# Kernel tuning notes

Hardware: AMD Instinct MI355X
Metric: run time of the kernel (lower is better)

Reference implementation:

```python
import jax, jax.numpy as jnp
import numpy as np

NB, HD, NL, NF = 5, 64, 4, 10           # num_bins, hidden_dim(d_model), num_layers, num_frames
DI, DS, DC, DTR = 128, 16, 4, 4          # d_inner=2*HD, d_state, d_conv, dt_rank=ceil(HD/16)
B, H, W = 4, 64, 64


def _conv2d(x, w, b):
    y = jax.lax.conv_general_dilated(x, w, (1, 1), 'SAME',
                                     dimension_numbers=('NCHW', 'OIHW', 'NCHW'))
    return y + b[None, :, None, None]


def _bn_relu(x, gamma, beta, eps=1e-5):
    # BatchNorm2d in training mode: biased batch stats over (N,H,W)
    mean = x.mean(axis=(0, 2, 3), keepdims=True)
    var = x.var(axis=(0, 2, 3), keepdims=True)
    y = (x - mean) * jax.lax.rsqrt(var + eps)
    return jax.nn.relu(y * gamma[None, :, None, None] + beta[None, :, None, None])


def _silu(x):
    return x * jax.nn.sigmoid(x)


def _causal_dwconv(x, w, b):
    # x: (B,L,DI), w: (DI,K) depthwise causal conv, b: (DI,)
    K = w.shape[1]
    L = x.shape[1]
    xp = jnp.pad(x, ((0, 0), (K - 1, 0), (0, 0)))
    y = sum(xp[:, k:k + L, :] * w[:, k] for k in range(K))
    return y + b


def _selective_scan(u, delta, A, Bm, Cm, D):
    # u,delta: (B,L,DI); A: (DI,DS); Bm,Cm: (B,L,DS); D: (DI,)
    dT, BT, CT, uT = (t.transpose(1, 0, 2) for t in (delta, Bm, Cm, u))
    h0 = jnp.zeros((u.shape[0], A.shape[0], A.shape[1]), u.dtype)

    def step(h, inp):
        d_t, B_t, C_t, u_t = inp                     # (B,DI),(B,DS),(B,DS),(B,DI)
        dA = jnp.exp(d_t[:, :, None] * A)            # (B,DI,DS)
        h = dA * h + (d_t * u_t)[:, :, None] * B_t[:, None, :]
        y = jnp.einsum('bds,bs->bd', h, C_t)
        return h, y

    _, ys = jax.lax.scan(step, h0, (dT, BT, CT, uT))  # ys: (L,B,DI)
    return ys.transpose(1, 0, 2) + u * D


def _mamba(x, in_proj, conv_w, conv_b, x_proj, dt_w, dt_b, A_log, Dp, out_proj):
    xz = x @ in_proj.T                               # (B,L,2*DI)
    xi, z = jnp.split(xz, 2, axis=-1)
    xi = _silu(_causal_dwconv(xi, conv_w, conv_b))
    xdbc = xi @ x_proj.T                             # (B,L,DTR+2*DS)
    dt, Bm, Cm = jnp.split(xdbc, [DTR, DTR + DS], axis=-1)
    delta = jax.nn.softplus(dt @ dt_w.T + dt_b)
    A = -jnp.exp(A_log)
    y = _selective_scan(xi, delta, A, Bm, Cm, Dp)
    return (y * _silu(z)) @ out_proj.T


def setup_inputs() -> dict:
    key = jax.random.key(0)
    ks = jax.random.split(key, 20)
    s = 0.02
    inp = {
        'x': jax.random.normal(ks[0], (B, NB, H, W), jnp.float32),
        'enc_w': jax.random.normal(ks[1], (HD, NB, 3, 3), jnp.float32) * s,
        'enc_b': jnp.zeros((HD,), jnp.float32),
        'enc_g': jnp.ones((HD,), jnp.float32),
        'enc_be': jnp.zeros((HD,), jnp.float32),
        'in_proj': jax.random.normal(ks[2], (NL, 2 * DI, HD), jnp.float32) * s,
        'conv_w': jax.random.normal(ks[3], (NL, DI, DC), jnp.float32) * s,
        'conv_b': jnp.zeros((NL, DI), jnp.float32),
        'x_proj': jax.random.normal(ks[4], (NL, DTR + 2 * DS, DI), jnp.float32) * s,
        'dt_w': jax.random.normal(ks[5], (NL, DI, DTR), jnp.float32) * s,
        'dt_b': jax.random.normal(ks[6], (NL, DI), jnp.float32) * 0.1 - 4.0,
        'A_log': jnp.broadcast_to(jnp.log(jnp.arange(1, DS + 1, dtype=jnp.float32)),
                                  (NL, DI, DS)).copy(),
        'Dp': jnp.ones((NL, DI), jnp.float32),
        'out_proj': jax.random.normal(ks[7], (NL, HD, DI), jnp.float32) * s,
        'dec1_w': jax.random.normal(ks[8], (HD, HD, 3, 3), jnp.float32) * s,
        'dec1_b': jnp.zeros((HD,), jnp.float32),
        'dec1_g': jnp.ones((HD,), jnp.float32),
        'dec1_be': jnp.zeros((HD,), jnp.float32),
        'dec2_w': jax.random.normal(ks[9], (NF, HD, 3, 3), jnp.float32) * s,
        'dec2_b': jnp.zeros((NF,), jnp.float32),
    }
    return inp


def reference(x, enc_w, enc_b, enc_g, enc_be, in_proj, conv_w, conv_b, x_proj,
              dt_w, dt_b, A_log, Dp, out_proj, dec1_w, dec1_b, dec1_g, dec1_be,
              dec2_w, dec2_b):
    Bb, _, Hh, Ww = x.shape
    h = _bn_relu(_conv2d(x, enc_w, enc_b), enc_g, enc_be)   # (B,HD,H,W)
    t = h.reshape(Bb, HD, Hh * Ww).transpose(0, 2, 1)        # (B,L,HD)
    for i in range(NL):
        t = t + _mamba(t, in_proj[i], conv_w[i], conv_b[i], x_proj[i],
                       dt_w[i], dt_b[i], A_log[i], Dp[i], out_proj[i])
    h = t.transpose(0, 2, 1).reshape(Bb, HD, Hh, Ww)
    h = _bn_relu(_conv2d(h, dec1_w, dec1_b), dec1_g, dec1_be)
    return _conv2d(h, dec2_w, dec2_b)                        # (B,NF,H,W)
```

## Files before the change

kernel.cpp:

```cpp
#include <hip/hip_runtime.h>
#include <hip/hip_bf16.h>

#define BB   4
#define NBC  5
#define HD   64
#define NLAYER 4
#define NFC  10
#define DIM  128
#define DSN  16
#define DCN  4
#define DTRK 4
#define HH   64
#define WWD  64
#define LL   4096
#define MM   (BB*LL)
#define NCHUNK 128
#define CLEN   32

__global__ void k_prep_all(const float* __restrict__ in_proj, const float* __restrict__ out_proj,
                           const float* __restrict__ dec1_w, const float* __restrict__ dec2_w,
                           float* __restrict__ wTin, float* __restrict__ wTout,
                           float* __restrict__ wT1, float* __restrict__ wT2,
                           float* __restrict__ stats, float* __restrict__ stats2) {
    int idx = blockIdx.x * blockDim.x + threadIdx.x;
    if (idx < 65536) {
        int n = idx & 255, k = (idx >> 8) & 63, l = idx >> 14;
        wTin[idx] = in_proj[(l << 14) + (n << 6) + k];
    } else if (idx < 98304) {
        int j = idx - 65536;
        int n = j & 63, k = (j >> 6) & 127, l = j >> 13;
        wTout[j] = out_proj[(l << 13) + (n << 7) + k];
    } else if (idx < 135168) {
        int j = idx - 98304;
        int co = j & 63, tap = (j >> 6) % 9, ci = j / 576;
        wT1[j] = dec1_w[co * 576 + ci * 9 + tap];
    } else if (idx < 142848) {
        int j = idx - 135168;
        int tap = j % 12, t2 = j / 12, co = t2 % NFC, ci = t2 / NFC;
        wT2[j] = (tap < 9) ? dec2_w[co * 576 + ci * 9 + tap] : 0.f;
    } else if (idx < 143104) {
        int j = idx - 142848;
        if (j < 128) stats[j] = 0.f; else stats2[j - 128] = 0.f;
    }
}

__global__ void k_enc_conv(const float* __restrict__ x, const float* __restrict__ w,
                           const float* __restrict__ bias, float* __restrict__ out,
                           float* __restrict__ stats) {
    __shared__ float r1[256], r2[256];
    int tid = threadIdx.x;
    int idx = blockIdx.x * 256 + tid;
    int wx = idx & 63;
    int hy = (idx >> 6) & 63;
    int co = (idx >> 12) & 63;
    int b  = idx >> 18;
    float acc = bias[co];
    for (int ci = 0; ci < NBC; ++ci) {
        const float* xin = x + (((long)(b * NBC + ci)) << 12);
        const float* wp  = w + (co * NBC + ci) * 9;
        #pragma unroll
        for (int kh = 0; kh < 3; ++kh) {
            int ih = hy + kh - 1;
            if (ih < 0 || ih >= HH) continue;
            #pragma unroll
            for (int kw = 0; kw < 3; ++kw) {
                int iw = wx + kw - 1;
                if (iw < 0 || iw >= WWD) continue;
                acc += xin[(ih << 6) + iw] * wp[kh * 3 + kw];
            }
        }
    }
    out[idx] = acc;
    r1[tid] = acc; r2[tid] = acc * acc;
    __syncthreads();
    for (int off = 128; off > 0; off >>= 1) {
        if (tid < off) { r1[tid] += r1[tid + off]; r2[tid] += r2[tid + off]; }
        __syncthreads();
    }
    if (tid == 0) {
        atomicAdd(&stats[co], r1[0]);
        atomicAdd(&stats[64 + co], r2[0]);
    }
}

__global__ __launch_bounds__(256, 1) void k_gemm_in_bn(const float* __restrict__ src,
                                                       const float* __restrict__ stats,
                                                       const float* __restrict__ g,
                                                       const float* __restrict__ be,
                                                       const float* __restrict__ wT,
                                                       float* __restrict__ tout,
                                                       float* __restrict__ xz) {
    __shared__ __align__(16) float ts[64 * 68];
    __shared__ float sc[64], sh[64];
    long m0 = (long)blockIdx.x << 6;
    int b = (int)(m0 >> 12);
    int hw0 = (int)(m0 & 4095);
    int tid = threadIdx.x;
    if (tid < 64) {
        float m = stats[tid] * (1.f / 16384.f);
        float var = stats[64 + tid] * (1.f / 16384.f) - m * m;
        float ss = g[tid] * rsqrtf(var + 1e-5f);
        sc[tid] = ss; sh[tid] = be[tid] - m * ss;
    }
    __syncthreads();
    for (int i = tid; i < 4096; i += 256) {
        int pix = i & 63, c = i >> 6;
        float v = src[(((long)((b << 6) + c)) << 12) + hw0 + pix];
        ts[pix * 68 + c] = fmaxf(v * sc[c] + sh[c], 0.f);
    }
    __syncthreads();
    for (int i = tid; i < 4096; i += 256) {
        int r = i >> 6, c = i & 63;
        tout[(m0 + r) * 64 + c] = ts[r * 68 + c];
    }
    int rg = tid >> 5;
    int cg = tid & 31;
    float acc[8][8] = {};
    int n0 = cg << 3;
    for (int k4 = 0; k4 < 16; ++k4) {
        float4 a[8];
        #pragma unroll
        for (int r2 = 0; r2 < 8; ++r2)
            a[r2] = *(const float4*)&ts[((rg << 3) + r2) * 68 + (k4 << 2)];
        #pragma unroll
        for (int kk = 0; kk < 4; ++kk) {
            const float* wr = wT + (((k4 << 2) + kk) << 8) + n0;
            float4 w0 = *(const float4*)&wr[0];
            float4 w1 = *(const float4*)&wr[4];
            #pragma unroll
            for (int r2 = 0; r2 < 8; ++r2) {
                float av = (kk == 0) ? a[r2].x : (kk == 1) ? a[r2].y
                         : (kk == 2) ? a[r2].z : a[r2].w;
                acc[r2][0] += av * w0.x; acc[r2][1] += av * w0.y;
                acc[r2][2] += av * w0.z; acc[r2][3] += av * w0.w;
                acc[r2][4] += av * w1.x; acc[r2][5] += av * w1.y;
                acc[r2][6] += av * w1.z; acc[r2][7] += av * w1.w;
            }
        }
    }
    #pragma unroll
    for (int r2 = 0; r2 < 8; ++r2) {
        long m = m0 + (rg << 3) + r2;
        *(float4*)&xz[(m << 8) + n0]     = make_float4(acc[r2][0], acc[r2][1], acc[r2][2], acc[r2][3]);
        *(float4*)&xz[(m << 8) + n0 + 4] = make_float4(acc[r2][4], acc[r2][5], acc[r2][6], acc[r2][7]);
    }
}

__global__ __launch_bounds__(256, 2) void k_xproj_fused(
        const float* __restrict__ xz, const float* __restrict__ cw,
        const float* __restrict__ cb, const float* __restrict__ Wx,
        const float* __restrict__ dw, const float* __restrict__ dbias,
        const float* __restrict__ A_log,
        float* __restrict__ xi, float* __restrict__ xdbc,
        float* __restrict__ delta, float* __restrict__ Pb, float* __restrict__ Sb) {
    __shared__ float xz_s[35 * 132];
    __shared__ float xi_s[32 * 132];
    __shared__ float w_s[36 * 132];
    __shared__ float xs[32 * 40];
    __shared__ float cwT[4 * 128];
    __shared__ float cb_s[128];
    long m0 = (long)blockIdx.x << 5;
    int l0 = (int)(m0 & 4095);
    int b = (int)(m0 >> 12);
    int chunk = l0 >> 5;
    int tid = threadIdx.x;

    for (int i = tid; i < 35 * 128; i += 256) {
        int j = i >> 7, k = i & 127;
        int l = l0 - 3 + j;
        float v = 0.f;
        if (l >= 0) v = xz[(m0 - 3 + j) * 256 + k];
        xz_s[j * 132 + k] = v;
    }
    if (tid < 128) cb_s[tid] = cb[tid];
    for (int i = tid; i < 512; i += 256) {
        int kk = i >> 7, di = i & 127;
        cwT[(kk << 7) + di] = cw[(di << 2) + kk];
    }
    for (int i = tid; i < 4608; i += 256) {
        int n = i >> 7, k = i & 127;
        w_s[n * 132 + k] = Wx[i];
    }
    __syncthreads();

    for (int ii = 0; ii < 4; ++ii) {
        int i = tid + (ii << 8);
        int r = i >> 5;
        int d4 = (i & 31) << 2;
        float4 a = *(const float4*)&cb_s[d4];
        #pragma unroll
        for (int kk = 0; kk < 4; ++kk) {
            float4 xv = *(const float4*)&xz_s[(r + kk) * 132 + d4];
            float4 wv = *(const float4*)&cwT[(kk << 7) + d4];
            a.x += xv.x * wv.x; a.y += xv.y * wv.y;
            a.z += xv.z * wv.z; a.w += xv.w * wv.w;
        }
        a.x = a.x / (1.f + __expf(-a.x));
        a.y = a.y / (1.f + __expf(-a.y));
        a.z = a.z / (1.f + __expf(-a.z));
        a.w = a.w / (1.f + __expf(-a.w));
        *(float4*)&xi_s[r * 132 + d4] = a;
        *(float4*)&xi[(m0 + r) * 128 + d4] = a;
    }
    __syncthreads();

    int n = tid & 63;
    int rg = tid >> 6;
    if (n < 36) {
        float acc[8] = {0,0,0,0,0,0,0,0};
        for (int k4 = 0; k4 < 32; ++k4) {
            float4 w4 = *(const float4*)&w_s[n * 132 + (k4 << 2)];
            #pragma unroll
            for (int r = 0; r < 8; ++r) {
                float4 a4 = *(const float4*)&xi_s[((rg << 3) + r) * 132 + (k4 << 2)];
                acc[r] += a4.x * w4.x + a4.y * w4.y + a4.z * w4.z + a4.w * w4.w;
            }
        }
        #pragma unroll
        for (int r = 0; r < 8; ++r) {
            int rr = (rg << 3) + r;
            xdbc[(m0 + rr) * 36 + n] = acc[r];
            xs[rr * 40 + n] = acc[r];
        }
    }
    __syncthreads();

    float* delta_s = xz_s;
    for (int i = tid; i < 4096; i += 256) {
        int r = i >> 7, di = i & 127;
        float v = dbias[di];
        float4 d4 = *(const float4*)&dw[di << 2];
        v += xs[r * 40 + 0] * d4.x + xs[r * 40 + 1] * d4.y
           + xs[r * 40 + 2] * d4.z + xs[r * 40 + 3] * d4.w;
        float sp = (v > 20.f) ? v : log1pf(expf(v));
        delta[(m0 + r) * 128 + di] = sp;
        delta_s[r * 132 + di] = sp;
    }
    __syncthreads();

    {
        int di = tid >> 1;
        int dso = (tid & 1) << 3;
        float4 al0 = *(const float4*)&A_log[(di << 4) + dso];
        float4 al1 = *(const float4*)&A_log[(di << 4) + dso + 4];
        float Av[8] = { -expf(al0.x), -expf(al0.y), -expf(al0.z), -expf(al0.w),
                        -expf(al1.x), -expf(al1.y), -expf(al1.z), -expf(al1.w) };
        float h[8] = {0,0,0,0,0,0,0,0};
        float P[8] = {1,1,1,1,1,1,1,1};
        #pragma unroll 4
        for (int i = 0; i < CLEN; ++i) {
            float d = delta_s[i * 132 + di];
            float u = xi_s[i * 132 + di];
            float du = d * u;
            float4 B0 = *(float4*)&xs[i * 40 + DTRK + dso];
            float4 B1 = *(float4*)&xs[i * 40 + DTRK + dso + 4];
            float a0 = __expf(d * Av[0]); h[0] = a0 * h[0] + du * B0.x; P[0] *= a0;
            float a1 = __expf(d * Av[1]); h[1] = a1 * h[1] + du * B0.y; P[1] *= a1;
            float a2 = __expf(d * Av[2]); h[2] = a2 * h[2] + du * B0.z; P[2] *= a2;
            float a3 = __expf(d * Av[3]); h[3] = a3 * h[3] + du * B0.w; P[3] *= a3;
            float a4 = __expf(d * Av[4]); h[4] = a4 * h[4] + du * B1.x; P[4] *= a4;
            float a5 = __expf(d * Av[5]); h[5] = a5 * h[5] + du * B1.y; P[5] *= a5;
            float a6 = __expf(d * Av[6]); h[6] = a6 * h[6] + du * B1.z; P[6] *= a6;
            float a7 = __expf(d * Av[7]); h[7] = a7 * h[7] + du * B1.w; P[7] *= a7;
        }
        long o = (((long)chunk * BB + b) << 11) + (di << 4) + dso;
        *(float4*)&Pb[o]     = make_float4(P[0], P[1], P[2], P[3]);
        *(float4*)&Pb[o + 4] = make_float4(P[4], P[5], P[6], P[7]);
        *(float4*)&Sb[o]     = make_float4(h[0], h[1], h[2], h[3]);
        *(float4*)&Sb[o + 4] = make_float4(h[4], h[5], h[6], h[7]);
    }
}

__global__ void k_scan_p2(float* Pb, const float* __restrict__ Sb) {
    int t = blockIdx.x * blockDim.x + threadIdx.x;
    int b = t >> 11;
    int s = t & 2047;
    float h = 0.f;
    for (int c = 0; c < NCHUNK; ++c) {
        long idx = (((long)c * BB + b) << 11) + s;
        float p = Pb[idx];
        float sv = Sb[idx];
        Pb[idx] = h;
        h = p * h + sv;
    }
}

__global__ __launch_bounds__(256, 1) void k_scan_p3_oi(
        const float* __restrict__ delta, const float* __restrict__ xi,
        const float* __restrict__ xdbc, const float* __restrict__ A_log,
        const float* __restrict__ Dp, const float* __restrict__ xz,
        const float* __restrict__ hin, const float* __restrict__ wTo,
        const float* __restrict__ wTi, float* __restrict__ tio,
        float* __restrict__ xz_out, int doB) {
    __shared__ __align__(16) float d_s[32 * 132];
    __shared__ __align__(16) float u_s[32 * 132];
    __shared__ __align__(16) float bc_s[32 * 36];
    __shared__ __align__(16) float t_s[32 * 68];
    int chunk = blockIdx.x, b = blockIdx.y;
    int tid = threadIdx.x;
    long t0 = ((long)b << 12) + (long)chunk * CLEN;

    for (int i = tid; i < 1024; i += 256) {
        int r = i >> 5, c4 = (i & 31) << 2;
        *(float4*)&d_s[r * 132 + c4] = *(const float4*)&delta[(t0 + r) * 128 + c4];
        *(float4*)&u_s[r * 132 + c4] = *(const float4*)&xi[(t0 + r) * 128 + c4];
    }
    {
        int r = tid >> 3, c4 = (tid & 7) << 2;
        *(float4*)&bc_s[r * 36 + c4] = *(const float4*)&xdbc[(t0 + r) * 36 + DTRK + c4];
    }

    int di = tid >> 1;
    int dso = (tid & 1) << 3;
    float4 al0 = *(const float4*)&A_log[(di << 4) + dso];
    float4 al1 = *(const float4*)&A_log[(di << 4) + dso + 4];
    float Av[8] = { -expf(al0.x), -expf(al0.y), -expf(al0.z), -expf(al0.w),
                    -expf(al1.x), -expf(al1.y), -expf(al1.z), -expf(al1.w) };
    float Dv = Dp[di];
    long o = (((long)chunk * BB + b) << 11) + (di << 4) + dso;
    float4 h0 = *(const float4*)&hin[o];
    float4 h1 = *(const float4*)&hin[o + 4];
    float h[8] = { h0.x, h0.y, h0.z, h0.w, h1.x, h1.y, h1.z, h1.w };
    __syncthreads();

    #pragma unroll 4
    for (int i = 0; i < CLEN; ++i) {
        float d = d_s[i * 132 + di];
        float u = u_s[i * 132 + di];
        float du = d * u;
        const float* bc = &bc_s[i * 36];
        float4 B0 = *(const float4*)&bc[dso];
        float4 B1 = *(const float4*)&bc[dso + 4];
        float4 C0 = *(const float4*)&bc[16 + dso];
        float4 C1 = *(const float4*)&bc[16 + dso + 4];
        float a0 = __expf(d * Av[0]); h[0] = a0 * h[0] + du * B0.x;
        float a1 = __expf(d * Av[1]); h[1] = a1 * h[1] + du * B0.y;
        float a2 = __expf(d * Av[2]); h[2] = a2 * h[2] + du * B0.z;
        float a3 = __expf(d * Av[3]); h[3] = a3 * h[3] + du * B0.w;
        float a4 = __expf(d * Av[4]); h[4] = a4 * h[4] + du * B1.x;
        float a5 = __expf(d * Av[5]); h[5] = a5 * h[5] + du * B1.y;
        float a6 = __expf(d * Av[6]); h[6] = a6 * h[6] + du * B1.z;
        float a7 = __expf(d * Av[7]); h[7] = a7 * h[7] + du * B1.w;
        float yp = h[0] * C0.x + h[1] * C0.y + h[2] * C0.z + h[3] * C0.w
                 + h[4] * C1.x + h[5] * C1.y + h[6] * C1.z + h[7] * C1.w;
        yp += __shfl_xor(yp, 1);
        if (dso == 0)
            u_s[i * 132 + di] = yp + u * Dv;
    }
    __syncthreads();

    for (int i = tid; i < 1024; i += 256) {
        int r = i >> 5, c4 = (i & 31) << 2;
        float4 y4 = *(float4*)&u_s[r * 132 + c4];
        float4 z4 = *(const float4*)&xz[((t0 + r) << 8) + DIM + c4];
        y4.x *= z4.x / (1.f + __expf(-z4.x));
        y4.y *= z4.y / (1.f + __expf(-z4.y));
        y4.z *= z4.z / (1.f + __expf(-z4.z));
        y4.w *= z4.w / (1.f + __expf(-z4.w));
        *(float4*)&u_s[r * 132 + c4] = y4;
    }
    __syncthreads();

    {
        int rg = tid >> 4, cg = tid & 15;
        int n0 = cg << 2;
        float acc[2][4] = {};
        for (int k4 = 0; k4 < 32; ++k4) {
            float4 a0 = *(const float4*)&u_s[(rg << 1) * 132 + (k4 << 2)];
            float4 a1 = *(const float4*)&u_s[((rg << 1) + 1) * 132 + (k4 << 2)];
            #pragma unroll
            for (int kk = 0; kk < 4; ++kk) {
                const float* wr = wTo + (((k4 << 2) + kk) << 6) + n0;
                float4 w0 = *(const float4*)&wr[0];
                float av0 = (kk == 0) ? a0.x : (kk == 1) ? a0.y : (kk == 2) ? a0.z : a0.w;
                float av1 = (kk == 0) ? a1.x : (kk == 1) ? a1.y : (kk == 2) ? a1.z : a1.w;
                acc[0][0] += av0 * w0.x; acc[0][1] += av0 * w0.y;
                acc[0][2] += av0 * w0.z; acc[0][3] += av0 * w0.w;
                acc[1][0] += av1 * w0.x; acc[1][1] += av1 * w0.y;
                acc[1][2] += av1 * w0.z; acc[1][3] += av1 * w0.w;
            }
        }
        #pragma unroll
        for (int r2 = 0; r2 < 2; ++r2) {
            long m = t0 + (rg << 1) + r2;
            float4 tv = *(const float4*)&tio[(m << 6) + n0];
            tv.x += acc[r2][0]; tv.y += acc[r2][1];
            tv.z += acc[r2][2]; tv.w += acc[r2][3];
            *(float4*)&tio[(m << 6) + n0] = tv;
            *(float4*)&t_s[((rg << 1) + r2) * 68 + n0] = tv;
        }
    }
    if (!doB) return;
    __syncthreads();

    {
        int rg = tid >> 5, cgn = tid & 31;
        int n0 = cgn << 3;
        float acc[4][8] = {};
        for (int k4 = 0; k4 < 16; ++k4) {
            float4 a[4];
            #pragma unroll
            for (int r2 = 0; r2 < 4; ++r2)
                a[r2] = *(const float4*)&t_s[((rg << 2) + r2) * 68 + (k4 << 2)];
            #pragma unroll
            for (int kk = 0; kk < 4; ++kk) {
                const float* wr = wTi + (((k4 << 2) + kk) << 8) + n0;
                float4 w0 = *(const float4*)&wr[0];
                float4 w1 = *(const float4*)&wr[4];
                #pragma unroll
                for (int r2 = 0; r2 < 4; ++r2) {
                    float av = (kk == 0) ? a[r2].x : (kk == 1) ? a[r2].y
                             : (kk == 2) ? a[r2].z : a[r2].w;
                    acc[r2][0] += av * w0.x; acc[r2][1] += av * w0.y;
                    acc[r2][2] += av * w0.z; acc[r2][3] += av * w0.w;
                    acc[r2][4] += av * w1.x; acc[r2][5] += av * w1.y;
                    acc[r2][6] += av * w1.z; acc[r2][7] += av * w1.w;
                }
            }
        }
        #pragma unroll
        for (int r2 = 0; r2 < 4; ++r2) {
            long m = t0 + (rg << 2) + r2;
            *(float4*)&xz_out[(m << 8) + n0]     = make_float4(acc[r2][0], acc[r2][1], acc[r2][2], acc[r2][3]);
            *(float4*)&xz_out[(m << 8) + n0 + 4] = make_float4(acc[r2][4], acc[r2][5], acc[r2][6], acc[r2][7]);
        }
    }
}

__global__ __launch_bounds__(256, 1) void k_dec1_new(const float* __restrict__ tin,
                                                     const float* __restrict__ wT,
                                                     const float* __restrict__ bias,
                                                     float* __restrict__ out,
                                                     float* __restrict__ stats2) {
    __shared__ __align__(16) float x_s[64 * 132];
    __shared__ __align__(16) float w_s[4 * 4608];
    int tile = blockIdx.x;
    int b = blockIdx.y;
    int ty0 = (tile >> 3) << 3;
    int tx0 = (tile & 7) << 3;
    int tid = threadIdx.x;
    int wv = tid >> 6;
    int lane = tid & 63;
    int r = lane >> 3;
    int cg = lane & 7;

    for (int i = tid; i < 6400; i += 256) {
        int pl = i >> 6;
        int c = i & 63;
        int py = pl / 10, px = pl - py * 10;
        int ih = ty0 + py - 1, iw = tx0 + px - 1;
        float v = 0.f;
        if (ih >= 0 && ih < HH && iw >= 0 && iw < WWD)
            v = tin[(((long)((b << 12) + (ih << 6) + iw)) << 6) + c];
        x_s[c * 132 + py * 12 + px] = v;
    }
    float* myw = &w_s[wv * 4608];
    const float* gw = wT + (wv * 16) * 576;
    float4 pref[18];
    #pragma unroll
    for (int i = 0; i < 18; ++i)
        pref[i] = *(const float4*)&gw[(i * 64 + lane) * 4];
    #pragma unroll
    for (int i = 0; i < 18; ++i)
        *(float4*)&myw[(i * 64 + lane) * 4] = pref[i];
    __syncthreads();

    float acc[8][8] = {};
    #pragma unroll
    for (int ch = 0; ch < 2; ++ch) {
        if (ch == 0) {
            const float* gw1 = wT + (wv * 16 + 8) * 576;
            #pragma unroll
            for (int i = 0; i < 18; ++i)
                pref[i] = *(const float4*)&gw1[(i * 64 + lane) * 4];
        }
        for (int cl = 0; cl < 8; ++cl) {
            int cib = wv * 16 + ch * 8 + cl;
            float xrow[3][10];
            #pragma unroll
            for (int kh = 0; kh < 3; ++kh) {
                const float* xr = &x_s[cib * 132 + (r + kh) * 12];
                float4 a0 = *(const float4*)&xr[0];
                float4 a1 = *(const float4*)&xr[4];
                float2 a2 = *(const float2*)&xr[8];
                xrow[kh][0] = a0.x; xrow[kh][1] = a0.y; xrow[kh][2] = a0.z; xrow[kh][3] = a0.w;
                xrow[kh][4] = a1.x; xrow[kh][5] = a1.y; xrow[kh][6] = a1.z; xrow[kh][7] = a1.w;
                xrow[kh][8] = a2.x; xrow[kh][9] = a2.y;
            }
            const float* wp = &myw[cl * 576];
            #pragma unroll
            for (int kh = 0; kh < 3; ++kh) {
                #pragma unroll
                for (int kw = 0; kw < 3; ++kw) {
                    const float* wp2 = wp + (kh * 3 + kw) * 64 + (cg << 3);
                    float4 wa = *(const float4*)&wp2[0];
                    float4 wb = *(const float4*)&wp2[4];
                    #pragma unroll
                    for (int j = 0; j < 8; ++j) {
                        float xv = xrow[kh][kw + j];
                        acc[j][0] += xv * wa.x; acc[j][1] += xv * wa.y;
                        acc[j][2] += xv * wa.z; acc[j][3] += xv * wa.w;
                        acc[j][4] += xv * wb.x; acc[j][5] += xv * wb.y;
                        acc[j][6] += xv * wb.z; acc[j][7] += xv * wb.w;
                    }
                }
            }
        }
        if (ch == 0) {
            #pragma unroll
            for (int i = 0; i < 18; ++i)
                *(float4*)&myw[(i * 64 + lane) * 4] = pref[i];
        }
    }

    #pragma unroll
    for (int j = 0; j < 8; ++j) {
        *(float4*)&myw[lane * 68 + (j << 3)]     = make_float4(acc[j][0], acc[j][1], acc[j][2], acc[j][3]);
        *(float4*)&myw[lane * 68 + (j << 3) + 4] = make_float4(acc[j][4], acc[j][5], acc[j][6], acc[j][7]);
    }
    __syncthreads();

    float bv = bias[lane];
    float ssum = 0.f, ssq = 0.f;
    #pragma unroll
    for (int pp = 0; pp < 16; ++pp) {
        int pr = (wv << 1) + (pp >> 3);
        int pc = pp & 7;
        int ol = (pr << 3) + (lane >> 3);
        int ix = (pc << 3) + (lane & 7);
        float s = w_s[ol * 68 + ix] + w_s[4608 + ol * 68 + ix]
                + w_s[9216 + ol * 68 + ix] + w_s[13824 + ol * 68 + ix] + bv;
        out[(((long)((b << 12) + ((ty0 + pr) << 6) + tx0 + pc)) << 6) + lane] = s;
        ssum += s; ssq += s * s;
    }
    float* red = x_s;
    red[(wv << 6) + lane] = ssum;
    red[256 + (wv << 6) + lane] = ssq;
    __syncthreads();
    if (tid < 64) {
        float a = red[tid] + red[64 + tid] + red[128 + tid] + red[192 + tid];
        float q = red[256 + tid] + red[320 + tid] + red[384 + tid] + red[448 + tid];
        atomicAdd(&stats2[tid], a);
        atomicAdd(&stats2[64 + tid], q);
    }
}

__global__ void k_dec2_fused(const float* __restrict__ src, const float* __restrict__ stats2,
                             const float* __restrict__ g, const float* __restrict__ be,
                             const float* __restrict__ wT, const float* __restrict__ bias,
                             float* __restrict__ out) {
    __shared__ float x_s[64 * 101];
    __shared__ float w_s[64 * NFC * 12];
    __shared__ float sc_s[64];
    __shared__ float sh_s[64];
    int tile = blockIdx.x;
    int b = blockIdx.y;
    int ty0 = (tile >> 3) << 3;
    int tx0 = (tile & 7) << 3;
    int tid = threadIdx.x;

    if (tid < 64) {
        float m = stats2[tid] * (1.f / 16384.f);
        float var = stats2[64 + tid] * (1.f / 16384.f) - m * m;
        float s = g[tid] * rsqrtf(var + 1e-5f);
        sc_s[tid] = s;
        sh_s[tid] = be[tid] - m * s;
    }
    for (int i = tid; i < 64 * NFC * 12; i += 256)
        w_s[i] = wT[i];
    __syncthreads();

    for (int i = tid; i < 6400; i += 256) {
        int pl = i >> 6;
        int c = i & 63;
        int py = pl / 10, px = pl - py * 10;
        int ih = ty0 + py - 1, iw = tx0 + px - 1;
        float v = 0.f;
        if (ih >= 0 && ih < HH && iw >= 0 && iw < WWD) {
            v = src[((long)((b << 12) + (ih << 6) + iw)) * 64 + c];
            v = fmaxf(v * sc_s[c] + sh_s[c], 0.f);
        }
        x_s[c * 101 + pl] = v;
    }
    __syncthreads();

    int px = tid & 63;
    int py = px >> 3, pxx = px & 7;
    int cog = tid >> 6;
    float acc[3] = {0.f, 0.f, 0.f};
    int nco = (cog < 2) ? 3 : 2;

    for (int ci = 0; ci < 64; ++ci) {
        const float* xr = &x_s[ci * 101 + py * 10 + pxx];
        float xv[9];
        #pragma unroll
        for (int kh = 0; kh < 3; ++kh)
            #pragma unroll
            for (int kw = 0; kw < 3; ++kw)
                xv[kh * 3 + kw] = xr[kh * 10 + kw];
        #pragma unroll
        for (int j = 0; j < 3; ++j) {
            if (j >= nco) break;
            int co = cog + (j << 2);
            const float* wp = &w_s[(ci * NFC + co) * 12];
            float4 w0 = *(const float4*)&wp[0];
            float4 w1 = *(const float4*)&wp[4];
            float  w8 = wp[8];
            acc[j] += xv[0] * w0.x + xv[1] * w0.y + xv[2] * w0.z + xv[3] * w0.w
                    + xv[4] * w1.x + xv[5] * w1.y + xv[6] * w1.z + xv[7] * w1.w
                    + xv[8] * w8;
        }
    }
    int hw = ((ty0 + py) << 6) + tx0 + pxx;
    #pragma unroll
    for (int j = 0; j < 3; ++j) {
        if (j >= nco) break;
        int co = cog + (j << 2);
        out[((long)(b * NFC + co) << 12) + hw] = acc[j] + bias[co];
    }
}

extern "C" void kernel_launch(void* const* d_in, const int* in_sizes, int n_in,
                              void* d_out, int out_size, void* d_ws, size_t ws_size,
                              hipStream_t stream) {
    const float* x       = (const float*)d_in[0];
    const float* enc_w   = (const float*)d_in[1];
    const float* enc_b   = (const float*)d_in[2];
    const float* enc_g   = (const float*)d_in[3];
    const float* enc_be  = (const float*)d_in[4];
    const float* in_proj = (const float*)d_in[5];
    const float* conv_w  = (const float*)d_in[6];
    const float* conv_b  = (const float*)d_in[7];
    const float* x_proj  = (const float*)d_in[8];
    const float* dt_w    = (const float*)d_in[9];
    const float* dt_b    = (const float*)d_in[10];
    const float* A_log   = (const float*)d_in[11];
    const float* Dp      = (const float*)d_in[12];
    const float* out_prj = (const float*)d_in[13];
    const float* dec1_w  = (const float*)d_in[14];
    const float* dec1_b  = (const float*)d_in[15];
    const float* dec1_g  = (const float*)d_in[16];
    const float* dec1_be = (const float*)d_in[17];
    const float* dec2_w  = (const float*)d_in[18];
    const float* dec2_b  = (const float*)d_in[19];
    float* out = (float*)d_out;

    float* ws = (float*)d_ws;
    size_t off = 0;
    float* conv_buf  = ws + off; off += 1048576;
    float* stats     = ws + off; off += 128;
    float* stats2    = ws + off; off += 128;
    float* wT1       = ws + off; off += 36864;
    float* wT2       = ws + off; off += 7680;
    float* wTin      = ws + off; off += 65536;
    float* wTout     = ws + off; off += 32768;
    float* t_buf     = ws + off; off += 1048576;
    float* xz_buf    = ws + off; off += 4194304;
    float* xi_buf    = ws + off; off += 2097152;
    float* xdbc_buf  = ws + off; off += 589824;
    float* delta_buf = ws + off; off += 2097152;
    float* Sb_buf    = ws + off; off += 1048576;
    (void)ws_size; (void)in_sizes; (void)n_in; (void)out_size;

    float* Pb = conv_buf;
    float* Sb = Sb_buf;

    k_prep_all<<<560, 256, 0, stream>>>(in_proj, out_prj, dec1_w, dec2_w,
                                        wTin, wTout, wT1, wT2, stats, stats2);

    k_enc_conv<<<4096, 256, 0, stream>>>(x, enc_w, enc_b, conv_buf, stats);

    k_gemm_in_bn<<<256, 256, 0, stream>>>(conv_buf, stats, enc_g, enc_be, wTin, t_buf, xz_buf);
    dim3 pg(NCHUNK, BB);
    for (int i = 0; i < NLAYER; ++i) {
        k_xproj_fused<<<512, 256, 0, stream>>>(xz_buf, conv_w + i * DIM * DCN,
                                               conv_b + i * DIM, x_proj + i * 36 * DIM,
                                               dt_w + i * DIM * DTRK, dt_b + i * DIM,
                                               A_log + i * DIM * DSN,
                                               xi_buf, xdbc_buf, delta_buf, Pb, Sb);
        k_scan_p2<<<32, 256, 0, stream>>>(Pb, Sb);
        int doB = (i < NLAYER - 1) ? 1 : 0;
        k_scan_p3_oi<<<pg, 256, 0, stream>>>(delta_buf, xi_buf, xdbc_buf,
                                             A_log + i * DIM * DSN, Dp + i * DIM,
                                             xz_buf, Pb, wTout + i * 8192,
                                             wTin + ((i + 1) & 3) * 16384,
                                             t_buf, xz_buf, doB);
    }

    dim3 dg1(64, BB);
    k_dec1_new<<<dg1, 256, 0, stream>>>(t_buf, wT1, dec1_b, conv_buf, stats2);
    k_dec2_fused<<<dg1, 256, 0, stream>>>(conv_buf, stats2, dec1_g, dec1_be, wT2, dec2_b, out);
}
```

Measured before the change: 491.8 us.

## Fuse all Mamba layers into one persistent cooperative kernel with grid syncs

Replaces the per-layer three-kernel sequence (xproj+chunk scan, inter-chunk scan, output scan+projections) with a single cooperative kernel of 512 blocks that loops over the four layers and separates phases with grid-wide syncs. Each block keeps its chunk's xi, delta and B/C values in shared memory across phases instead of writing xi/delta/xdbc to global memory and re-reading them. This removes kernel launch overhead and global round trips. In exchange it relies on all 512 blocks being co-resident (two per CU at 256 threads), and the sequential inter-chunk scan now runs on only 32 blocks while the rest wait at a grid barrier.

```diff
diff --git a/kernel.cpp b/kernel.cpp
--- a/kernel.cpp
+++ b/kernel.cpp
@@ -1,5 +1,8 @@
 #include <hip/hip_runtime.h>
 #include <hip/hip_bf16.h>
+#include <hip/hip_cooperative_groups.h>
+
+namespace cg = cooperative_groups;
 
 #define BB   4
 #define NBC  5
@@ -146,283 +149,266 @@
     }
 }
 
-__global__ __launch_bounds__(256, 2) void k_xproj_fused(
-        const float* __restrict__ xz, const float* __restrict__ cw,
-        const float* __restrict__ cb, const float* __restrict__ Wx,
-        const float* __restrict__ dw, const float* __restrict__ dbias,
-        const float* __restrict__ A_log,
-        float* __restrict__ xi, float* __restrict__ xdbc,
-        float* __restrict__ delta, float* __restrict__ Pb, float* __restrict__ Sb) {
-    __shared__ float xz_s[35 * 132];
-    __shared__ float xi_s[32 * 132];
-    __shared__ float w_s[36 * 132];
-    __shared__ float xs[32 * 40];
-    __shared__ float cwT[4 * 128];
-    __shared__ float cb_s[128];
-    long m0 = (long)blockIdx.x << 5;
+__global__ __launch_bounds__(256, 2) void k_mamba_all(
+        float* __restrict__ xz,
+        const float* __restrict__ cw_all, const float* __restrict__ cb_all,
+        const float* __restrict__ Wx_all,
+        const float* __restrict__ dw_all, const float* __restrict__ dbias_all,
+        const float* __restrict__ Alog_all, const float* __restrict__ Dp_all,
+        const float* __restrict__ wTo_all, const float* __restrict__ wTi_all,
+        float* __restrict__ tio, float* Pb, float* Sb) {
+    cg::grid_group gg = cg::this_grid();
+    __shared__ __align__(16) float smem[15516];
+    float* xz_s = smem;
+    float* xi_s = smem + 4620;
+    float* w_s  = smem + 8844;
+    float* xs   = smem + 13596;
+    float* cwT  = smem + 14876;
+    float* cb_s = smem + 15388;
+
+    int bx = blockIdx.x;
+    int tid = threadIdx.x;
+    long m0 = (long)bx << 5;
     int l0 = (int)(m0 & 4095);
-    int b = (int)(m0 >> 12);
-    int chunk = l0 >> 5;
-    int tid = threadIdx.x;
-
-    for (int i = tid; i < 35 * 128; i += 256) {
-        int j = i >> 7, k = i & 127;
-        int l = l0 - 3 + j;
-        float v = 0.f;
-        if (l >= 0) v = xz[(m0 - 3 + j) * 256 + k];
-        xz_s[j * 132 + k] = v;
-    }
-    if (tid < 128) cb_s[tid] = cb[tid];
-    for (int i = tid; i < 512; i += 256) {
-        int kk = i >> 7, di = i & 127;
-        cwT[(kk << 7) + di] = cw[(di << 2) + kk];
-    }
-    for (int i = tid; i < 4608; i += 256) {
-        int n = i >> 7, k = i & 127;
-        w_s[n * 132 + k] = Wx[i];
-    }
-    __syncthreads();
-
-    for (int ii = 0; ii < 4; ++ii) {
-        int i = tid + (ii << 8);
-        int r = i >> 5;
-        int d4 = (i & 31) << 2;
-        float4 a = *(const float4*)&cb_s[d4];
-        #pragma unroll
-        for (int kk = 0; kk < 4; ++kk) {
-            float4 xv = *(const float4*)&xz_s[(r + kk) * 132 + d4];
-            float4 wv = *(const float4*)&cwT[(kk << 7) + d4];
-            a.x += xv.x * wv.x; a.y += xv.y * wv.y;
-            a.z += xv.z * wv.z; a.w += xv.w * wv.w;
-        }
-        a.x = a.x / (1.f + __expf(-a.x));
-        a.y = a.y / (1.f + __expf(-a.y));
-        a.z = a.z / (1.f + __expf(-a.z));
-        a.w = a.w / (1.f + __expf(-a.w));
-        *(float4*)&xi_s[r * 132 + d4] = a;
-        *(float4*)&xi[(m0 + r) * 128 + d4] = a;
-    }
-    __syncthreads();
-
-    int n = tid & 63;
-    int rg = tid >> 6;
-    if (n < 36) {
-        float acc[8] = {0,0,0,0,0,0,0,0};
-        for (int k4 = 0; k4 < 32; ++k4) {
-            float4 w4 = *(const float4*)&w_s[n * 132 + (k4 << 2)];
-            #pragma unroll
-            for (int r = 0; r < 8; ++r) {
-                float4 a4 = *(const float4*)&xi_s[((rg << 3) + r) * 132 + (k4 << 2)];
-                acc[r] += a4.x * w4.x + a4.y * w4.y + a4.z * w4.z + a4.w * w4.w;
-            }
-        }
-        #pragma unroll
-        for (int r = 0; r < 8; ++r) {
-            int rr = (rg << 3) + r;
-            xdbc[(m0 + rr) * 36 + n] = acc[r];
-            xs[rr * 40 + n] = acc[r];
-        }
-    }
-    __syncthreads();
-
+    int b = bx >> 7;
+    int chunk = bx & 127;
+    int di = tid >> 1;
+    int dso = (tid & 1) << 3;
     float* delta_s = xz_s;
-    for (int i = tid; i < 4096; i += 256) {
-        int r = i >> 7, di = i & 127;
-        float v = dbias[di];
-        float4 d4 = *(const float4*)&dw[di << 2];
-        v += xs[r * 40 + 0] * d4.x + xs[r * 40 + 1] * d4.y
-           + xs[r * 40 + 2] * d4.z + xs[r * 40 + 3] * d4.w;
-        float sp = (v > 20.f) ? v : log1pf(expf(v));
-        delta[(m0 + r) * 128 + di] = sp;
-        delta_s[r * 132 + di] = sp;
-    }
-    __syncthreads();
-
-    {
-        int di = tid >> 1;
-        int dso = (tid & 1) << 3;
+
+    for (int L = 0; L < NLAYER; ++L) {
+        const float* cw    = cw_all + L * DIM * DCN;
+        const float* cbp   = cb_all + L * DIM;
+        const float* Wx    = Wx_all + L * 36 * DIM;
+        const float* dw    = dw_all + L * DIM * DTRK;
+        const float* dbias = dbias_all + L * DIM;
+        const float* A_log = Alog_all + L * DIM * DSN;
+        const float* wTo   = wTo_all + L * 8192;
+        const float* wTi   = wTi_all + ((L + 1) & 3) * 16384;
+
+        for (int i = tid; i < 35 * 128; i += 256) {
+            int j = i >> 7, k = i & 127;
+            int l = l0 - 3 + j;
+            float v = 0.f;
+            if (l >= 0) v = xz[(m0 - 3 + j) * 256 + k];
+            xz_s[j * 132 + k] = v;
+        }
+        if (tid < 128) cb_s[tid] = cbp[tid];
+        for (int i = tid; i < 512; i += 256) {
+            int kk = i >> 7, dd = i & 127;
+            cwT[(kk << 7) + dd] = cw[(dd << 2) + kk];
+        }
+        for (int i = tid; i < 4608; i += 256) {
+            int nn = i >> 7, k = i & 127;
+            w_s[nn * 132 + k] = Wx[i];
+        }
+        __syncthreads();
+
+        for (int ii = 0; ii < 4; ++ii) {
+            int i = tid + (ii << 8);
+            int r = i >> 5;
+            int d4 = (i & 31) << 2;
+            float4 a = *(const float4*)&cb_s[d4];
+            #pragma unroll
+            for (int kk = 0; kk < 4; ++kk) {
+                float4 xv = *(const float4*)&xz_s[(r + kk) * 132 + d4];
+                float4 wv = *(const float4*)&cwT[(kk << 7) + d4];
+                a.x += xv.x * wv.x; a.y += xv.y * wv.y;
+                a.z += xv.z * wv.z; a.w += xv.w * wv.w;
+            }
+            a.x = a.x / (1.f + __expf(-a.x));
+            a.y = a.y / (1.f + __expf(-a.y));
+            a.z = a.z / (1.f + __expf(-a.z));
+            a.w = a.w / (1.f + __expf(-a.w));
+            *(float4*)&xi_s[r * 132 + d4] = a;
+        }
+        __syncthreads();
+
+        {
+            int n = tid & 63;
+            int rg = tid >> 6;
+            if (n < 36) {
+                float acc[8] = {0,0,0,0,0,0,0,0};
+                for (int k4 = 0; k4 < 32; ++k4) {
+                    float4 w4 = *(const float4*)&w_s[n * 132 + (k4 << 2)];
+                    #pragma unroll
+                    for (int r = 0; r < 8; ++r) {
+                        float4 a4 = *(const float4*)&xi_s[((rg << 3) + r) * 132 + (k4 << 2)];
+                        acc[r] += a4.x * w4.x + a4.y * w4.y + a4.z * w4.z + a4.w * w4.w;
+                    }
+                }
+                #pragma unroll
+                for (int r = 0; r < 8; ++r)
+                    xs[((rg << 3) + r) * 40 + n] = acc[r];
+            }
+        }
+        __syncthreads();
+
+        for (int i = tid; i < 4096; i += 256) {
+            int r = i >> 7, dd = i & 127;
+            float v = dbias[dd];
+            float4 d4 = *(const float4*)&dw[dd << 2];
+            v += xs[r * 40 + 0] * d4.x + xs[r * 40 + 1] * d4.y
+               + xs[r * 40 + 2] * d4.z + xs[r * 40 + 3] * d4.w;
+            delta_s[r * 132 + dd] = (v > 20.f) ? v : log1pf(expf(v));
+        }
+        __syncthreads();
+
         float4 al0 = *(const float4*)&A_log[(di << 4) + dso];
         float4 al1 = *(const float4*)&A_log[(di << 4) + dso + 4];
         float Av[8] = { -expf(al0.x), -expf(al0.y), -expf(al0.z), -expf(al0.w),
                         -expf(al1.x), -expf(al1.y), -expf(al1.z), -expf(al1.w) };
-        float h[8] = {0,0,0,0,0,0,0,0};
-        float P[8] = {1,1,1,1,1,1,1,1};
-        #pragma unroll 4
-        for (int i = 0; i < CLEN; ++i) {
-            float d = delta_s[i * 132 + di];
-            float u = xi_s[i * 132 + di];
-            float du = d * u;
-            float4 B0 = *(float4*)&xs[i * 40 + DTRK + dso];
-            float4 B1 = *(float4*)&xs[i * 40 + DTRK + dso + 4];
-            float a0 = __expf(d * Av[0]); h[0] = a0 * h[0] + du * B0.x; P[0] *= a0;
-            float a1 = __expf(d * Av[1]); h[1] = a1 * h[1] + du * B0.y; P[1] *= a1;
-            float a2 = __expf(d * Av[2]); h[2] = a2 * h[2] + du * B0.z; P[2] *= a2;
-            float a3 = __expf(d * Av[3]); h[3] = a3 * h[3] + du * B0.w; P[3] *= a3;
-            float a4 = __expf(d * Av[4]); h[4] = a4 * h[4] + du * B1.x; P[4] *= a4;
-            float a5 = __expf(d * Av[5]); h[5] = a5 * h[5] + du * B1.y; P[5] *= a5;
-            float a6 = __expf(d * Av[6]); h[6] = a6 * h[6] + du * B1.z; P[6] *= a6;
-            float a7 = __expf(d * Av[7]); h[7] = a7 * h[7] + du * B1.w; P[7] *= a7;
-        }
         long o = (((long)chunk * BB + b) << 11) + (di << 4) + dso;
-        *(float4*)&Pb[o]     = make_float4(P[0], P[1], P[2], P[3]);
-        *(float4*)&Pb[o + 4] = make_float4(P[4], P[5], P[6], P[7]);
-        *(float4*)&Sb[o]     = make_float4(h[0], h[1], h[2], h[3]);
-        *(float4*)&Sb[o + 4] = make_float4(h[4], h[5], h[6], h[7]);
-    }
-}
-
-__global__ void k_scan_p2(float* Pb, const float* __restrict__ Sb) {
-    int t = blockIdx.x * blockDim.x + threadIdx.x;
-    int b = t >> 11;
-    int s = t & 2047;
-    float h = 0.f;
-    for (int c = 0; c < NCHUNK; ++c) {
-        long idx = (((long)c * BB + b) << 11) + s;
-        float p = Pb[idx];
-        float sv = Sb[idx];
-        Pb[idx] = h;
-        h = p * h + sv;
-    }
-}
-
-__global__ __launch_bounds__(256, 1) void k_scan_p3_oi(
-        const float* __restrict__ delta, const float* __restrict__ xi,
-        const float* __restrict__ xdbc, const float* __restrict__ A_log,
-        const float* __restrict__ Dp, const float* __restrict__ xz,
-        const float* __restrict__ hin, const float* __restrict__ wTo,
-        const float* __restrict__ wTi, float* __restrict__ tio,
-        float* __restrict__ xz_out, int doB) {
-    __shared__ __align__(16) float d_s[32 * 132];
-    __shared__ __align__(16) float u_s[32 * 132];
-    __shared__ __align__(16) float bc_s[32 * 36];
-    __shared__ __align__(16) float t_s[32 * 68];
-    int chunk = blockIdx.x, b = blockIdx.y;
-    int tid = threadIdx.x;
-    long t0 = ((long)b << 12) + (long)chunk * CLEN;
-
-    for (int i = tid; i < 1024; i += 256) {
-        int r = i >> 5, c4 = (i & 31) << 2;
-        *(float4*)&d_s[r * 132 + c4] = *(const float4*)&delta[(t0 + r) * 128 + c4];
-        *(float4*)&u_s[r * 132 + c4] = *(const float4*)&xi[(t0 + r) * 128 + c4];
-    }
-    {
-        int r = tid >> 3, c4 = (tid & 7) << 2;
-        *(float4*)&bc_s[r * 36 + c4] = *(const float4*)&xdbc[(t0 + r) * 36 + DTRK + c4];
-    }
-
-    int di = tid >> 1;
-    int dso = (tid & 1) << 3;
-    float4 al0 = *(const float4*)&A_log[(di << 4) + dso];
-    float4 al1 = *(const float4*)&A_log[(di << 4) + dso + 4];
-    float Av[8] = { -expf(al0.x), -expf(al0.y), -expf(al0.z), -expf(al0.w),
-                    -expf(al1.x), -expf(al1.y), -expf(al1.z), -expf(al1.w) };
-    float Dv = Dp[di];
-    long o = (((long)chunk * BB + b) << 11) + (di << 4) + dso;
-    float4 h0 = *(const float4*)&hin[o];
-    float4 h1 = *(const float4*)&hin[o + 4];
-    float h[8] = { h0.x, h0.y, h0.z, h0.w, h1.x, h1.y, h1.z, h1.w };
-    __syncthreads();
-
-    #pragma unroll 4
-    for (int i = 0; i < CLEN; ++i) {
-        float d = d_s[i * 132 + di];
-        float u = u_s[i * 132 + di];
-        float du = d * u;
-        const float* bc = &bc_s[i * 36];
-        float4 B0 = *(const float4*)&bc[dso];
-        float4 B1 = *(const float4*)&bc[dso + 4];
-        float4 C0 = *(const float4*)&bc[16 + dso];
-        float4 C1 = *(const float4*)&bc[16 + dso + 4];
-        float a0 = __expf(d * Av[0]); h[0] = a0 * h[0] + du * B0.x;
-        float a1 = __expf(d * Av[1]); h[1] = a1 * h[1] + du * B0.y;
-        float a2 = __expf(d * Av[2]); h[2] = a2 * h[2] + du * B0.z;
-        float a3 = __expf(d * Av[3]); h[3] = a3 * h[3] + du * B0.w;
-        float a4 = __expf(d * Av[4]); h[4] = a4 * h[4] + du * B1.x;
-        float a5 = __expf(d * Av[5]); h[5] = a5 * h[5] + du * B1.y;
-        float a6 = __expf(d * Av[6]); h[6] = a6 * h[6] + du * B1.z;
-        float a7 = __expf(d * Av[7]); h[7] = a7 * h[7] + du * B1.w;
-        float yp = h[0] * C0.x + h[1] * C0.y + h[2] * C0.z + h[3] * C0.w
-                 + h[4] * C1.x + h[5] * C1.y + h[6] * C1.z + h[7] * C1.w;
-        yp += __shfl_xor(yp, 1);
-        if (dso == 0)
-            u_s[i * 132 + di] = yp + u * Dv;
-    }
-    __syncthreads();
-
-    for (int i = tid; i < 1024; i += 256) {
-        int r = i >> 5, c4 = (i & 31) << 2;
-        float4 y4 = *(float4*)&u_s[r * 132 + c4];
-        float4 z4 = *(const float4*)&xz[((t0 + r) << 8) + DIM + c4];
-        y4.x *= z4.x / (1.f + __expf(-z4.x));
-        y4.y *= z4.y / (1.f + __expf(-z4.y));
-        y4.z *= z4.z / (1.f + __expf(-z4.z));
-        y4.w *= z4.w / (1.f + __expf(-z4.w));
-        *(float4*)&u_s[r * 132 + c4] = y4;
-    }
-    __syncthreads();
-
-    {
-        int rg = tid >> 4, cg = tid & 15;
-        int n0 = cg << 2;
-        float acc[2][4] = {};
-        for (int k4 = 0; k4 < 32; ++k4) {
-            float4 a0 = *(const float4*)&u_s[(rg << 1) * 132 + (k4 << 2)];
-            float4 a1 = *(const float4*)&u_s[((rg << 1) + 1) * 132 + (k4 << 2)];
-            #pragma unroll
-            for (int kk = 0; kk < 4; ++kk) {
-                const float* wr = wTo + (((k4 << 2) + kk) << 6) + n0;
-                float4 w0 = *(const float4*)&wr[0];
-                float av0 = (kk == 0) ? a0.x : (kk == 1) ? a0.y : (kk == 2) ? a0.z : a0.w;
-                float av1 = (kk == 0) ? a1.x : (kk == 1) ? a1.y : (kk == 2) ? a1.z : a1.w;
-                acc[0][0] += av0 * w0.x; acc[0][1] += av0 * w0.y;
-                acc[0][2] += av0 * w0.z; acc[0][3] += av0 * w0.w;
-                acc[1][0] += av1 * w0.x; acc[1][1] += av1 * w0.y;
-                acc[1][2] += av1 * w0.z; acc[1][3] += av1 * w0.w;
-            }
-        }
-        #pragma unroll
-        for (int r2 = 0; r2 < 2; ++r2) {
-            long m = t0 + (rg << 1) + r2;
-            float4 tv = *(const float4*)&tio[(m << 6) + n0];
-            tv.x += acc[r2][0]; tv.y += acc[r2][1];
-            tv.z += acc[r2][2]; tv.w += acc[r2][3];
-            *(float4*)&tio[(m << 6) + n0] = tv;
-            *(float4*)&t_s[((rg << 1) + r2) * 68 + n0] = tv;
-        }
-    }
-    if (!doB) return;
-    __syncthreads();
-
-    {
-        int rg = tid >> 5, cgn = tid & 31;
-        int n0 = cgn << 3;
-        float acc[4][8] = {};
-        for (int k4 = 0; k4 < 16; ++k4) {
-            float4 a[4];
-            #pragma unroll
-            for (int r2 = 0; r2 < 4; ++r2)
-                a[r2] = *(const float4*)&t_s[((rg << 2) + r2) * 68 + (k4 << 2)];
-            #pragma unroll
-            for (int kk = 0; kk < 4; ++kk) {
-                const float* wr = wTi + (((k4 << 2) + kk) << 8) + n0;
-                float4 w0 = *(const float4*)&wr[0];
-                float4 w1 = *(const float4*)&wr[4];
+
+        {
+            float h[8] = {0,0,0,0,0,0,0,0};
+            float P[8] = {1,1,1,1,1,1,1,1};
+            #pragma unroll 4
+            for (int i = 0; i < CLEN; ++i) {
+                float d = delta_s[i * 132 + di];
+                float u = xi_s[i * 132 + di];
+                float du = d * u;
+                float4 B0 = *(float4*)&xs[i * 40 + 4 + dso];
+                float4 B1 = *(float4*)&xs[i * 40 + 8 + dso];
+                float a0 = __expf(d * Av[0]); h[0] = a0 * h[0] + du * B0.x; P[0] *= a0;
+                float a1 = __expf(d * Av[1]); h[1] = a1 * h[1] + du * B0.y; P[1] *= a1;
+                float a2 = __expf(d * Av[2]); h[2] = a2 * h[2] + du * B0.z; P[2] *= a2;
+                float a3 = __expf(d * Av[3]); h[3] = a3 * h[3] + du * B0.w; P[3] *= a3;
+                float a4 = __expf(d * Av[4]); h[4] = a4 * h[4] + du * B1.x; P[4] *= a4;
+                float a5 = __expf(d * Av[5]); h[5] = a5 * h[5] + du * B1.y; P[5] *= a5;
+                float a6 = __expf(d * Av[6]); h[6] = a6 * h[6] + du * B1.z; P[6] *= a6;
+                float a7 = __expf(d * Av[7]); h[7] = a7 * h[7] + du * B1.w; P[7] *= a7;
+            }
+            *(float4*)&Pb[o]     = make_float4(P[0], P[1], P[2], P[3]);
+            *(float4*)&Pb[o + 4] = make_float4(P[4], P[5], P[6], P[7]);
+            *(float4*)&Sb[o]     = make_float4(h[0], h[1], h[2], h[3]);
+            *(float4*)&Sb[o + 4] = make_float4(h[4], h[5], h[6], h[7]);
+        }
+        gg.sync();
+
+        {
+            int flat = (bx << 8) + tid;
+            if (flat < 8192) {
+                int bb = flat >> 11;
+                int s = flat & 2047;
+                float h = 0.f;
+                for (int c = 0; c < NCHUNK; ++c) {
+                    long idx = (((long)c * BB + bb) << 11) + s;
+                    float p = Pb[idx];
+                    float sv = Sb[idx];
+                    Pb[idx] = h;
+                    h = p * h + sv;
+                }
+            }
+        }
+        gg.sync();
+
+        {
+            float Dv = Dp_all[L * DIM + di];
+            float4 h0 = *(const float4*)&Pb[o];
+            float4 h1 = *(const float4*)&Pb[o + 4];
+            float h[8] = { h0.x, h0.y, h0.z, h0.w, h1.x, h1.y, h1.z, h1.w };
+            #pragma unroll 4
+            for (int i = 0; i < CLEN; ++i) {
+                float d = delta_s[i * 132 + di];
+                float u = xi_s[i * 132 + di];
+                float du = d * u;
+                float4 B0 = *(const float4*)&xs[i * 40 + 4 + dso];
+                float4 B1 = *(const float4*)&xs[i * 40 + 8 + dso];
+                float4 C0 = *(const float4*)&xs[i * 40 + 20 + dso];
+                float4 C1 = *(const float4*)&xs[i * 40 + 24 + dso];
+                float a0 = __expf(d * Av[0]); h[0] = a0 * h[0] + du * B0.x;
+                float a1 = __expf(d * Av[1]); h[1] = a1 * h[1] + du * B0.y;
+                float a2 = __expf(d * Av[2]); h[2] = a2 * h[2] + du * B0.z;
+                float a3 = __expf(d * Av[3]); h[3] = a3 * h[3] + du * B0.w;
+                float a4 = __expf(d * Av[4]); h[4] = a4 * h[4] + du * B1.x;
+                float a5 = __expf(d * Av[5]); h[5] = a5 * h[5] + du * B1.y;
+                float a6 = __expf(d * Av[6]); h[6] = a6 * h[6] + du * B1.z;
+                float a7 = __expf(d * Av[7]); h[7] = a7 * h[7] + du * B1.w;
+                float yp = h[0] * C0.x + h[1] * C0.y + h[2] * C0.z + h[3] * C0.w
+                         + h[4] * C1.x + h[5] * C1.y + h[6] * C1.z + h[7] * C1.w;
+                yp += __shfl_xor(yp, 1);
+                if (dso == 0)
+                    xi_s[i * 132 + di] = yp + u * Dv;
+            }
+        }
+        __syncthreads();
+
+        for (int i = tid; i < 1024; i += 256) {
+            int r = i >> 5, c4 = (i & 31) << 2;
+            float4 y4 = *(float4*)&xi_s[r * 132 + c4];
+            float4 z4 = *(const float4*)&xz[((m0 + r) << 8) + DIM + c4];
+            y4.x *= z4.x / (1.f + __expf(-z4.x));
+            y4.y *= z4.y / (1.f + __expf(-z4.y));
+            y4.z *= z4.z / (1.f + __expf(-z4.z));
+            y4.w *= z4.w / (1.f + __expf(-z4.w));
+            *(float4*)&xi_s[r * 132 + c4] = y4;
+        }
+        __syncthreads();
+
+        float* t_s = w_s;
+        {
+            int rg = tid >> 4, cgc = tid & 15;
+            int n0 = cgc << 2;
+            float acc[2][4] = {};
+            for (int k4 = 0; k4 < 32; ++k4) {
+                float4 a0 = *(const float4*)&xi_s[(rg << 1) * 132 + (k4 << 2)];
+                float4 a1 = *(const float4*)&xi_s[((rg << 1) + 1) * 132 + (k4 << 2)];
                 #pragma unroll
-                for (int r2 = 0; r2 < 4; ++r2) {
-                    float av = (kk == 0) ? a[r2].x : (kk == 1) ? a[r2].y
-                             : (kk == 2) ? a[r2].z : a[r2].w;
-                    acc[r2][0] += av * w0.x; acc[r2][1] += av * w0.y;
-                    acc[r2][2] += av * w0.z; acc[r2][3] += av * w0.w;
-                    acc[r2][4] += av * w1.x; acc[r2][5] += av * w1.y;
-                    acc[r2][6] += av * w1.z; acc[r2][7] += av * w1.w;
+                for (int kk = 0; kk < 4; ++kk) {
+                    const float* wr = wTo + (((k4 << 2) + kk) << 6) + n0;
+                    float4 w0 = *(const float4*)&wr[0];
+                    float av0 = (kk == 0) ? a0.x : (kk == 1) ? a0.y : (kk == 2) ? a0.z : a0.w;
+                    float av1 = (kk == 0) ? a1.x : (kk == 1) ? a1.y : (kk == 2) ? a1.z : a1.w;
+                    acc[0][0] += av0 * w0.x; acc[0][1] += av0 * w0.y;
+                    acc[0][2] += av0 * w0.z; acc[0][3] += av0 * w0.w;
+                    acc[1][0] += av1 * w0.x; acc[1][1] += av1 * w0.y;
+                    acc[1][2] += av1 * w0.z; acc[1][3] += av1 * w0.w;
                 }
             }
-        }
-        #pragma unroll
-        for (int r2 = 0; r2 < 4; ++r2) {
-            long m = t0 + (rg << 2) + r2;
-            *(float4*)&xz_out[(m << 8) + n0]     = make_float4(acc[r2][0], acc[r2][1], acc[r2][2], acc[r2][3]);
-            *(float4*)&xz_out[(m << 8) + n0 + 4] = make_float4(acc[r2][4], acc[r2][5], acc[r2][6], acc[r2][7]);
+            #pragma unroll
+            for (int r2 = 0; r2 < 2; ++r2) {
+                long m = m0 + (rg << 1) + r2;
+                float4 tv = *(const float4*)&tio[(m << 6) + n0];
+                tv.x += acc[r2][0]; tv.y += acc[r2][1];
+                tv.z += acc[r2][2]; tv.w += acc[r2][3];
+                *(float4*)&tio[(m << 6) + n0] = tv;
+                *(float4*)&t_s[((rg << 1) + r2) * 68 + n0] = tv;
+            }
+        }
+        if (L < NLAYER - 1) {
+            __syncthreads();
+            int rg = tid >> 5, cgn = tid & 31;
+            int n0 = cgn << 3;
+            float acc[4][8] = {};
+            for (int k4 = 0; k4 < 16; ++k4) {
+                float4 a[4];
+                #pragma unroll
+                for (int r2 = 0; r2 < 4; ++r2)
+                    a[r2] = *(const float4*)&t_s[((rg << 2) + r2) * 68 + (k4 << 2)];
+                #pragma unroll
+                for (int kk = 0; kk < 4; ++kk) {
+                    const float* wr = wTi + (((k4 << 2) + kk) << 8) + n0;
+                    float4 w0 = *(const float4*)&wr[0];
+                    float4 w1 = *(const float4*)&wr[4];
+                    #pragma unroll
+                    for (int r2 = 0; r2 < 4; ++r2) {
+                        float av = (kk == 0) ? a[r2].x : (kk == 1) ? a[r2].y
+                                 : (kk == 2) ? a[r2].z : a[r2].w;
+                        acc[r2][0] += av * w0.x; acc[r2][1] += av * w0.y;
+                        acc[r2][2] += av * w0.z; acc[r2][3] += av * w0.w;
+                        acc[r2][4] += av * w1.x; acc[r2][5] += av * w1.y;
+                        acc[r2][6] += av * w1.z; acc[r2][7] += av * w1.w;
+                    }
+                }
+            }
+            #pragma unroll
+            for (int r2 = 0; r2 < 4; ++r2) {
+                long m = m0 + (rg << 2) + r2;
+                *(float4*)&xz[(m << 8) + n0]     = make_float4(acc[r2][0], acc[r2][1], acc[r2][2], acc[r2][3]);
+                *(float4*)&xz[(m << 8) + n0 + 4] = make_float4(acc[r2][4], acc[r2][5], acc[r2][6], acc[r2][7]);
+            }
+            gg.sync();
         }
     }
 }
@@ -442,7 +428,7 @@
     int wv = tid >> 6;
     int lane = tid & 63;
     int r = lane >> 3;
-    int cg = lane & 7;
+    int cg2 = lane & 7;
 
     for (int i = tid; i < 6400; i += 256) {
         int pl = i >> 6;
@@ -492,7 +478,7 @@
             for (int kh = 0; kh < 3; ++kh) {
                 #pragma unroll
                 for (int kw = 0; kw < 3; ++kw) {
-                    const float* wp2 = wp + (kh * 3 + kw) * 64 + (cg << 3);
+                    const float* wp2 = wp + (kh * 3 + kw) * 64 + (cg2 << 3);
                     float4 wa = *(const float4*)&wp2[0];
                     float4 wb = *(const float4*)&wp2[4];
                     #pragma unroll
@@ -656,9 +642,6 @@
     float* wTout     = ws + off; off += 32768;
     float* t_buf     = ws + off; off += 1048576;
     float* xz_buf    = ws + off; off += 4194304;
-    float* xi_buf    = ws + off; off += 2097152;
-    float* xdbc_buf  = ws + off; off += 589824;
-    float* delta_buf = ws + off; off += 2097152;
     float* Sb_buf    = ws + off; off += 1048576;
     (void)ws_size; (void)in_sizes; (void)n_in; (void)out_size;
 
@@ -669,22 +652,15 @@
                                         wTin, wTout, wT1, wT2, stats, stats2);
 
     k_enc_conv<<<4096, 256, 0, stream>>>(x, enc_w, enc_b, conv_buf, stats);
-
     k_gemm_in_bn<<<256, 256, 0, stream>>>(conv_buf, stats, enc_g, enc_be, wTin, t_buf, xz_buf);
-    dim3 pg(NCHUNK, BB);
-    for (int i = 0; i < NLAYER; ++i) {
-        k_xproj_fused<<<512, 256, 0, stream>>>(xz_buf, conv_w + i * DIM * DCN,
-                                               conv_b + i * DIM, x_proj + i * 36 * DIM,
-                                               dt_w + i * DIM * DTRK, dt_b + i * DIM,
-                                               A_log + i * DIM * DSN,
-                                               xi_buf, xdbc_buf, delta_buf, Pb, Sb);
-        k_scan_p2<<<32, 256, 0, stream>>>(Pb, Sb);
-        int doB = (i < NLAYER - 1) ? 1 : 0;
-        k_scan_p3_oi<<<pg, 256, 0, stream>>>(delta_buf, xi_buf, xdbc_buf,
-                                             A_log + i * DIM * DSN, Dp + i * DIM,
-                                             xz_buf, Pb, wTout + i * 8192,
-                                             wTin + ((i + 1) & 3) * 16384,
-                                             t_buf, xz_buf, doB);
+
+    {
+        void* args[] = { (void*)&xz_buf, (void*)&conv_w, (void*)&conv_b, (void*)&x_proj,
+                         (void*)&dt_w, (void*)&dt_b, (void*)&A_log, (void*)&Dp,
+                         (void*)&wTout, (void*)&wTin, (void*)&t_buf,
+                         (void*)&Pb, (void*)&Sb };
+        hipLaunchCooperativeKernel((void*)k_mamba_all, dim3(512), dim3(256),
+                                   args, 0, stream);
     }
 
     dim3 dg1(64, BB);
```

New measurement: 1.199 ms. 144% more time.
